# Optimization experiments

Measured on AMD Instinct MI355X. Metric: run time of the kernel, lower is better.

Reference implementation:

```python
import jax, jax.numpy as jnp
import numpy as np

ALPHA = 0.2  # LeakyReLU negative slope


def setup_inputs() -> dict:
    key = jax.random.key(0)
    k1, k2, k3 = jax.random.split(key, 3)
    B, N, F_in, F_out = 8, 2048, 256, 256
    h = jax.random.normal(k1, (B, N, F_in), dtype=jnp.float32)
    adj = jax.random.randint(k2, (B, N, N), 0, 2, dtype=jnp.int32)
    # xavier_uniform for W [F_in, F_out]
    limit = float(np.sqrt(6.0 / (F_in + F_out)))
    W = jax.random.uniform(k3, (F_in, F_out), dtype=jnp.float32, minval=-limit, maxval=limit)
    return {"h": h, "adj": adj, "W": W}


def reference(h, adj, W):
    # h: [B,N,F_in], W: [F_in,F_out] -> Wh: [B,N,F_out]
    Wh = jnp.einsum('bnf,fo->bno', h, W)
    # (Wh_i + Wh_j).sum(-1) == s[p] + s[q] with s = Wh.sum(-1); avoids [B,N,N,F] tensor
    s = Wh.sum(axis=-1)  # [B,N]
    e = jax.nn.leaky_relu(s[:, :, None] + s[:, None, :], negative_slope=ALPHA)  # [B,N,N]
    e = jnp.where(adj == 0, -jnp.inf, e)
    alpha = jax.nn.softmax(e, axis=-1)  # masked softmax over neighbors
    # dropout is identity in eval mode
    h_prime = jnp.einsum('bpq,bqo->bpo', alpha, Wh)  # [B,N,F_out]
    return h_prime
```

## Files before the change

kernel.cpp:

```cpp
#include <hip/hip_runtime.h>
#include <hip/hip_bf16.h>
#include <stdint.h>

#define LEAKY_ALPHA 0.2f

using f32x4 = __attribute__((ext_vector_type(4))) float;
using u32x2 = __attribute__((ext_vector_type(2))) unsigned int;
using u32x4 = __attribute__((ext_vector_type(4))) unsigned int;
using i32x4 = __attribute__((ext_vector_type(4))) int;
using s16x8 = __attribute__((ext_vector_type(8))) short;

static __device__ __forceinline__ unsigned short f2bf(float x) {
  __hip_bfloat16 b = __float2bfloat16(x);
  return __builtin_bit_cast(unsigned short, b);
}

__global__ __launch_bounds__(256) void gat_prep(
    const float* __restrict__ W, __hip_bfloat16* __restrict__ WT,
    float* __restrict__ wsum)
{
  const int o = blockIdx.x;
  const int t = threadIdx.x;
  WT[o * 256 + t] = __float2bfloat16(W[t * 256 + o]);
  float u = W[o * 256 + t];
#pragma unroll
  for (int off = 1; off < 64; off <<= 1) u += __shfl_xor(u, off, 64);
  __shared__ float red[4];
  if ((t & 63) == 0) red[t >> 6] = u;
  __syncthreads();
  if (t == 0) wsum[o] = red[0] + red[1] + red[2] + red[3];
}

__global__ __launch_bounds__(256) void gat_wh2(
    const float* __restrict__ h, const __hip_bfloat16* __restrict__ WT,
    const float* __restrict__ wsum, __hip_bfloat16* __restrict__ WhT,
    float* __restrict__ s)
{
  const int b = blockIdx.x >> 5;
  const int q0 = (blockIdx.x & 31) * 64;
  const int t = threadIdx.x;
  const int wid = t >> 6, lane = t & 63;

  __shared__ __align__(16) unsigned char Bh[64 * 512];
  __shared__ __align__(16) unsigned char Aw[256 * 128];
  __shared__ __align__(16) float wsl[256];

  wsl[t] = wsum[t];
  __syncthreads();

  {
    const int q = t >> 2;
    const int fs = (t & 3) * 64;
    const float* hrow = h + ((size_t)(b * 2048 + q0 + q)) * 256 + fs;
    float sp = 0.f;
#pragma unroll
    for (int c = 0; c < 8; ++c) {
      const f32x4 a  = *(const f32x4*)&hrow[c * 8];
      const f32x4 bq = *(const f32x4*)&hrow[c * 8 + 4];
      const f32x4 wa = *(const f32x4*)&wsl[fs + c * 8];
      const f32x4 wb = *(const f32x4*)&wsl[fs + c * 8 + 4];
      sp += a[0]*wa[0] + a[1]*wa[1] + a[2]*wa[2] + a[3]*wa[3]
          + bq[0]*wb[0] + bq[1]*wb[1] + bq[2]*wb[2] + bq[3]*wb[3];
      u32x4 pk;
      pk[0] = (unsigned)f2bf(a[0])  | ((unsigned)f2bf(a[1])  << 16);
      pk[1] = (unsigned)f2bf(a[2])  | ((unsigned)f2bf(a[3])  << 16);
      pk[2] = (unsigned)f2bf(bq[0]) | ((unsigned)f2bf(bq[1]) << 16);
      pk[3] = (unsigned)f2bf(bq[2]) | ((unsigned)f2bf(bq[3]) << 16);
      const int boff = q * 512 + ((fs * 2 + c * 16) ^ ((q & 7) << 4));
      *(u32x4*)&Bh[boff] = pk;
    }
    sp += __shfl_xor(sp, 1, 64);
    sp += __shfl_xor(sp, 2, 64);
    if ((t & 3) == 0) s[b * 2048 + q0 + q] = sp;
  }

  f32x4 acc[4][4];
#pragma unroll
  for (int i = 0; i < 4; ++i)
#pragma unroll
    for (int j = 0; j < 4; ++j) acc[i][j] = (f32x4)(0.f);

  for (int it = 0; it < 4; ++it) {
    const int f0 = it * 64;
    __syncthreads();
#pragma unroll
    for (int j = 0; j < 8; ++j) {
      const int o = (t >> 3) + 32 * j;
      const int c = t & 7;
      const u32x4 v = *(const u32x4*)&WT[o * 256 + f0 + c * 8];
      *(u32x4*)&Aw[o * 128 + ((c * 16) ^ ((o & 7) << 4))] = v;
    }
    __syncthreads();
#pragma unroll
    for (int kt = 0; kt < 2; ++kt) {
      const int kb = kt * 64 + ((lane >> 4) << 4);
      s16x8 af[4], bf[4];
#pragma unroll
      for (int qt = 0; qt < 4; ++qt) {
        const int qr = qt * 16 + (lane & 15);
        af[qt] = *(const s16x8*)&Bh[qr * 512 + ((f0 * 2 + kb) ^ ((qr & 7) << 4))];
      }
#pragma unroll
      for (int ot = 0; ot < 4; ++ot) {
        const int orow = wid * 64 + ot * 16 + (lane & 15);
        bf[ot] = *(const s16x8*)&Aw[orow * 128 + (kb ^ ((orow & 7) << 4))];
      }
#pragma unroll
      for (int qt = 0; qt < 4; ++qt)
#pragma unroll
        for (int ot = 0; ot < 4; ++ot)
          acc[qt][ot] = __builtin_amdgcn_mfma_f32_16x16x32_bf16(
              af[qt], bf[ot], acc[qt][ot], 0, 0, 0);
    }
  }

  __hip_bfloat16* __restrict__ WhTb = WhT + (size_t)b * 256 * 2048;
#pragma unroll
  for (int qt = 0; qt < 4; ++qt)
#pragma unroll
    for (int ot = 0; ot < 4; ++ot) {
      const int o = wid * 64 + ot * 16 + (lane & 15);
      const int ql = q0 + qt * 16 + ((lane >> 4) << 2);
      u32x2 pk;
      pk[0] = (unsigned)f2bf(acc[qt][ot][0]) | ((unsigned)f2bf(acc[qt][ot][1]) << 16);
      pk[1] = (unsigned)f2bf(acc[qt][ot][2]) | ((unsigned)f2bf(acc[qt][ot][3]) << 16);
      *(u32x2*)&WhTb[(size_t)o * 2048 + ql] = pk;
    }
}

__global__ __launch_bounds__(512, 4) void gat_attn(
    const int* __restrict__ adj, const float* __restrict__ s,
    const __hip_bfloat16* __restrict__ WhT, float* __restrict__ out)
{
  const int N = 2048;
  const int bid = blockIdx.x;
  const int swz = (bid & 7) * 64 + (bid >> 3);
  const int b = swz >> 6;
  const int inner = swz & 63;
  const int p0 = (inner >> 1) * 64;
  const int o0 = (inner & 1) * 128;
  const int t = threadIdx.x;
  const int wid = t >> 6, lane = t & 63;

  __shared__ __align__(16) unsigned char Bs[2][128 * 128];
  __shared__ __align__(16) unsigned char Pt[2][64 * 128];
  __shared__ __align__(16) float red_sh[8];
  __shared__ __align__(16) float l_sh[64];

  const int sp_row = t >> 3;
  const int sq8 = (t & 7) * 8;
  const int* __restrict__ adjrow = adj + ((size_t)(b * N + p0 + sp_row)) * N;
  const float* __restrict__ sB = s + b * N;
  const __hip_bfloat16* __restrict__ WhTb =
      WhT + (size_t)b * 256 * 2048 + (size_t)o0 * 2048;
  const int ptoff = sp_row * 128 + (((t & 7) * 16) ^ ((sp_row & 7) << 4));

  const int so = t >> 3;
  const int q16 = t & 7;

  const int pg = wid >> 2;
  const int og = wid & 3;

  u32x4 breg[2];
#pragma unroll
  for (int c = 0; c < 2; ++c)
    breg[c] = *(const u32x4*)&WhTb[(size_t)(so + 64 * c) * 2048 + q16 * 8];
  i32x4 aE0 = *(const i32x4*)&adjrow[sq8];
  i32x4 aE1 = *(const i32x4*)&adjrow[sq8 + 4];
  f32x4 sE0 = *(const f32x4*)&sB[sq8];
  f32x4 sE1 = *(const f32x4*)&sB[sq8 + 4];
  i32x4 aO0 = *(const i32x4*)&adjrow[64 + sq8];
  i32x4 aO1 = *(const i32x4*)&adjrow[64 + sq8 + 4];
  f32x4 sO0 = *(const f32x4*)&sB[64 + sq8];
  f32x4 sO1 = *(const f32x4*)&sB[64 + sq8 + 4];

  const f32x4 s4 = *(const f32x4*)&sB[t * 4];
  float bm = fmaxf(fmaxf(s4[0], s4[1]), fmaxf(s4[2], s4[3]));
#pragma unroll
  for (int off = 1; off < 64; off <<= 1) bm = fmaxf(bm, __shfl_xor(bm, off, 64));
  if (lane == 0) red_sh[wid] = bm;
  const float s_p = sB[p0 + sp_row];
  __syncthreads();
  float smax = red_sh[0];
#pragma unroll
  for (int k = 1; k < 8; ++k) smax = fmaxf(smax, red_sh[k]);
  const float xm = s_p + smax;
  const float m_p = (xm > 0.f) ? xm : (LEAKY_ALPHA * xm);

  f32x4 acc[2][2];
#pragma unroll
  for (int pt = 0; pt < 2; ++pt)
#pragma unroll
    for (int ot = 0; ot < 2; ++ot) acc[pt][ot] = (f32x4)(0.f);
  float lacc = 0.f;

  auto phase = [&](int BI, int QQ, i32x4& A0, i32x4& A1, f32x4& S0, f32x4& S1)
      __attribute__((always_inline)) {
    float wv[8];
#pragma unroll
    for (int i = 0; i < 4; ++i) {
      const float x = s_p + S0[i];
      const float le = (x > 0.f) ? x : (LEAKY_ALPHA * x);
      const float w = __expf(le - m_p);
      wv[i] = (A0[i] != 0) ? w : 0.f;
      lacc += wv[i];
    }
#pragma unroll
    for (int i = 0; i < 4; ++i) {
      const float x = s_p + S1[i];
      const float le = (x > 0.f) ? x : (LEAKY_ALPHA * x);
      const float w = __expf(le - m_p);
      wv[4 + i] = (A1[i] != 0) ? w : 0.f;
      lacc += wv[4 + i];
    }
    {
      u32x4 pw;
#pragma unroll
      for (int k2 = 0; k2 < 4; ++k2)
        pw[k2] = (unsigned)f2bf(wv[2 * k2]) |
                 ((unsigned)f2bf(wv[2 * k2 + 1]) << 16);
      *(u32x4*)&Pt[BI][ptoff] = pw;
    }
#pragma unroll
    for (int c = 0; c < 2; ++c) {
      const int o = so + 64 * c;
      *(u32x4*)&Bs[BI][o * 128 + ((q16 * 16) ^ ((o & 7) << 4))] = breg[c];
    }
    if (QQ + 64 < N) {
#pragma unroll
      for (int c = 0; c < 2; ++c)
        breg[c] = *(const u32x4*)&WhTb[(size_t)(so + 64 * c) * 2048 +
                                       QQ + 64 + q16 * 8];
    }
    {
      const int qr = (QQ + 128 < N) ? (QQ + 128) : (N - 64);
      A0 = *(const i32x4*)&adjrow[qr + sq8];
      A1 = *(const i32x4*)&adjrow[qr + sq8 + 4];
      S0 = *(const f32x4*)&sB[qr + sq8];
      S1 = *(const f32x4*)&sB[qr + sq8 + 4];
    }
    asm volatile("s_waitcnt lgkmcnt(0)" ::: "memory");
    __builtin_amdgcn_s_barrier();
    asm volatile("" ::: "memory");
    {
      s16x8 afr[2][2], bfr[2][2];
#pragma unroll
      for (int pt = 0; pt < 2; ++pt)
#pragma unroll
        for (int kt = 0; kt < 2; ++kt) {
          const int pa = pg * 32 + pt * 16 + (lane & 15);
          const int kb = kt * 64 + ((lane >> 4) << 4);
          afr[pt][kt] = *(const s16x8*)&Pt[BI][pa * 128 + (kb ^ ((pa & 7) << 4))];
        }
#pragma unroll
      for (int ot = 0; ot < 2; ++ot)
#pragma unroll
        for (int kt = 0; kt < 2; ++kt) {
          const int ob = og * 32 + ot * 16 + (lane & 15);
          const int kb = kt * 64 + ((lane >> 4) << 4);
          bfr[ot][kt] = *(const s16x8*)&Bs[BI][ob * 128 + (kb ^ ((ob & 7) << 4))];
        }
#pragma unroll
      for (int pt = 0; pt < 2; ++pt)
#pragma unroll
        for (int ot = 0; ot < 2; ++ot)
#pragma unroll
          for (int kt = 0; kt < 2; ++kt)
            acc[pt][ot] = __builtin_amdgcn_mfma_f32_16x16x32_bf16(
                afr[pt][kt], bfr[ot][kt], acc[pt][ot], 0, 0, 0);
    }
  };

  for (int q0 = 0; q0 < N; q0 += 128) {
    phase(0, q0, aE0, aE1, sE0, sE1);
    phase(1, q0 + 64, aO0, aO1, sO0, sO1);
  }

  lacc += __shfl_xor(lacc, 1, 64);
  lacc += __shfl_xor(lacc, 2, 64);
  lacc += __shfl_xor(lacc, 4, 64);
  if ((t & 7) == 0) l_sh[sp_row] = lacc;
  __syncthreads();

#pragma unroll
  for (int pt = 0; pt < 2; ++pt) {
    const int pb = pg * 32 + pt * 16 + ((lane >> 4) << 2);
    const f32x4 lv = *(const f32x4*)&l_sh[pb];
    f32x4 inv;
#pragma unroll
    for (int r = 0; r < 4; ++r) inv[r] = 1.f / lv[r];
#pragma unroll
    for (int ot = 0; ot < 2; ++ot) {
      const int o = o0 + og * 32 + ot * 16 + (lane & 15);
#pragma unroll
      for (int r = 0; r < 4; ++r) {
        const int row = p0 + pb + r;
        out[((size_t)(b * N + row)) * 256 + o] = acc[pt][ot][r] * inv[r];
      }
    }
  }
}

extern "C" void kernel_launch(void* const* d_in, const int* in_sizes, int n_in,
                              void* d_out, int out_size, void* d_ws, size_t ws_size,
                              hipStream_t stream) {
  const float* h = (const float*)d_in[0];
  const int* adj = (const int*)d_in[1];
  const float* W = (const float*)d_in[2];
  float* out = (float*)d_out;

  char* ws = (char*)d_ws;
  __hip_bfloat16* WhT = (__hip_bfloat16*)ws;
  float* s = (float*)(ws + (size_t)8 * 1024 * 1024);
  __hip_bfloat16* WT = (__hip_bfloat16*)(ws + (size_t)8 * 1024 * 1024 + 65536);
  float* wsum = (float*)(ws + (size_t)8 * 1024 * 1024 + 65536 + 131072);

  gat_prep<<<256, 256, 0, stream>>>(W, WT, wsum);
  gat_wh2<<<256, 256, 0, stream>>>(h, WT, wsum, WhT, s);
  gat_attn<<<512, 512, 0, stream>>>(adj, s, WhT, out);
}
```

Before: 60.07 us.

## Store Wh in MFMA fragment-major layout and load B operands directly to registers

The projection kernel now writes Wh in a pre-swizzled fragment-major layout, so each lane's MFMA B-operand fragment is a contiguous 16-byte chunk. The attention kernel then loads B fragments straight from global memory into registers, prefetched one step ahead. This removes the shared-memory staging buffer, its stores and its LDS reads. The trade-off is more redundant global/L2 traffic, since each wave loads its own B fragments instead of sharing through LDS, plus higher register pressure.

```diff
diff --git a/kernel.cpp b/kernel.cpp
--- a/kernel.cpp
+++ b/kernel.cpp
@@ -33,7 +33,7 @@
 
 __global__ __launch_bounds__(256) void gat_wh2(
     const float* __restrict__ h, const __hip_bfloat16* __restrict__ WT,
-    const float* __restrict__ wsum, __hip_bfloat16* __restrict__ WhT,
+    const float* __restrict__ wsum, __hip_bfloat16* __restrict__ FM,
     float* __restrict__ s)
 {
   const int b = blockIdx.x >> 5;
@@ -114,23 +114,25 @@
     }
   }
 
-  __hip_bfloat16* __restrict__ WhTb = WhT + (size_t)b * 256 * 2048;
+  char* __restrict__ FMb = (char*)FM + (size_t)b * 1048576;
 #pragma unroll
   for (int qt = 0; qt < 4; ++qt)
 #pragma unroll
     for (int ot = 0; ot < 4; ++ot) {
-      const int o = wid * 64 + ot * 16 + (lane & 15);
-      const int ql = q0 + qt * 16 + ((lane >> 4) << 2);
+      const int i = wid * 4 + ot;
+      const int q = q0 + qt * 16 + ((lane >> 4) << 2);
+      const int c = q >> 5, qq = q & 31;
+      const int lam = (lane & 15) | (((qq >> 3) & 3) << 4);
       u32x2 pk;
       pk[0] = (unsigned)f2bf(acc[qt][ot][0]) | ((unsigned)f2bf(acc[qt][ot][1]) << 16);
       pk[1] = (unsigned)f2bf(acc[qt][ot][2]) | ((unsigned)f2bf(acc[qt][ot][3]) << 16);
-      *(u32x2*)&WhTb[(size_t)o * 2048 + ql] = pk;
+      *(u32x2*)(FMb + ((size_t)(i * 64 + c) * 64 + lam) * 16 + (qq & 4) * 2) = pk;
     }
 }
 
 __global__ __launch_bounds__(512, 4) void gat_attn(
     const int* __restrict__ adj, const float* __restrict__ s,
-    const __hip_bfloat16* __restrict__ WhT, float* __restrict__ out)
+    const __hip_bfloat16* __restrict__ FM, float* __restrict__ out)
 {
   const int N = 2048;
   const int bid = blockIdx.x;
@@ -142,7 +144,6 @@
   const int t = threadIdx.x;
   const int wid = t >> 6, lane = t & 63;
 
-  __shared__ __align__(16) unsigned char Bs[2][128 * 128];
   __shared__ __align__(16) unsigned char Pt[2][64 * 128];
   __shared__ __align__(16) float red_sh[8];
   __shared__ __align__(16) float l_sh[64];
@@ -151,20 +152,21 @@
   const int sq8 = (t & 7) * 8;
   const int* __restrict__ adjrow = adj + ((size_t)(b * N + p0 + sp_row)) * N;
   const float* __restrict__ sB = s + b * N;
-  const __hip_bfloat16* __restrict__ WhTb =
-      WhT + (size_t)b * 256 * 2048 + (size_t)o0 * 2048;
   const int ptoff = sp_row * 128 + (((t & 7) * 16) ^ ((sp_row & 7) << 4));
-
-  const int so = t >> 3;
-  const int q16 = t & 7;
 
   const int pg = wid >> 2;
   const int og = wid & 3;
-
-  u32x4 breg[2];
-#pragma unroll
-  for (int c = 0; c < 2; ++c)
-    breg[c] = *(const u32x4*)&WhTb[(size_t)(so + 64 * c) * 2048 + q16 * 8];
+  const int ibase = (o0 >> 4) + og * 2;
+  const char* __restrict__ FMb = (const char*)FM + (size_t)b * 1048576 + lane * 16;
+
+  u32x4 bE[2][2], bO[2][2];
+#pragma unroll
+  for (int ot = 0; ot < 2; ++ot)
+#pragma unroll
+    for (int kt = 0; kt < 2; ++kt) {
+      bE[ot][kt] = *(const u32x4*)(FMb + ((size_t)((ibase + ot) * 64 + kt) * 1024));
+      bO[ot][kt] = *(const u32x4*)(FMb + ((size_t)((ibase + ot) * 64 + 2 + kt) * 1024));
+    }
   i32x4 aE0 = *(const i32x4*)&adjrow[sq8];
   i32x4 aE1 = *(const i32x4*)&adjrow[sq8 + 4];
   f32x4 sE0 = *(const f32x4*)&sB[sq8];
@@ -194,8 +196,8 @@
     for (int ot = 0; ot < 2; ++ot) acc[pt][ot] = (f32x4)(0.f);
   float lacc = 0.f;
 
-  auto phase = [&](int BI, int QQ, i32x4& A0, i32x4& A1, f32x4& S0, f32x4& S1)
-      __attribute__((always_inline)) {
+  auto phase = [&](int BI, int QQ, i32x4& A0, i32x4& A1, f32x4& S0, f32x4& S1,
+                   u32x4 (&BF)[2][2]) __attribute__((always_inline)) {
     float wv[8];
 #pragma unroll
     for (int i = 0; i < 4; ++i) {
@@ -221,17 +223,6 @@
                  ((unsigned)f2bf(wv[2 * k2 + 1]) << 16);
       *(u32x4*)&Pt[BI][ptoff] = pw;
     }
-#pragma unroll
-    for (int c = 0; c < 2; ++c) {
-      const int o = so + 64 * c;
-      *(u32x4*)&Bs[BI][o * 128 + ((q16 * 16) ^ ((o & 7) << 4))] = breg[c];
-    }
-    if (QQ + 64 < N) {
-#pragma unroll
-      for (int c = 0; c < 2; ++c)
-        breg[c] = *(const u32x4*)&WhTb[(size_t)(so + 64 * c) * 2048 +
-                                       QQ + 64 + q16 * 8];
-    }
     {
       const int qr = (QQ + 128 < N) ? (QQ + 128) : (N - 64);
       A0 = *(const i32x4*)&adjrow[qr + sq8];
@@ -243,7 +234,7 @@
     __builtin_amdgcn_s_barrier();
     asm volatile("" ::: "memory");
     {
-      s16x8 afr[2][2], bfr[2][2];
+      s16x8 afr[2][2];
 #pragma unroll
       for (int pt = 0; pt < 2; ++pt)
 #pragma unroll
@@ -253,27 +244,29 @@
           afr[pt][kt] = *(const s16x8*)&Pt[BI][pa * 128 + (kb ^ ((pa & 7) << 4))];
         }
 #pragma unroll
-      for (int ot = 0; ot < 2; ++ot)
-#pragma unroll
-        for (int kt = 0; kt < 2; ++kt) {
-          const int ob = og * 32 + ot * 16 + (lane & 15);
-          const int kb = kt * 64 + ((lane >> 4) << 4);
-          bfr[ot][kt] = *(const s16x8*)&Bs[BI][ob * 128 + (kb ^ ((ob & 7) << 4))];
-        }
-#pragma unroll
       for (int pt = 0; pt < 2; ++pt)
 #pragma unroll
         for (int ot = 0; ot < 2; ++ot)
 #pragma unroll
           for (int kt = 0; kt < 2; ++kt)
             acc[pt][ot] = __builtin_amdgcn_mfma_f32_16x16x32_bf16(
-                afr[pt][kt], bfr[ot][kt], acc[pt][ot], 0, 0, 0);
+                afr[pt][kt], __builtin_bit_cast(s16x8, BF[ot][kt]),
+                acc[pt][ot], 0, 0, 0);
+    }
+    {
+      const int cr = ((QQ + 128 < N) ? (QQ + 128) : (N - 64)) >> 5;
+#pragma unroll
+      for (int ot = 0; ot < 2; ++ot)
+#pragma unroll
+        for (int kt = 0; kt < 2; ++kt)
+          BF[ot][kt] = *(const u32x4*)(FMb +
+              ((size_t)((ibase + ot) * 64 + cr + kt) * 1024));
     }
   };
 
   for (int q0 = 0; q0 < N; q0 += 128) {
-    phase(0, q0, aE0, aE1, sE0, sE1);
-    phase(1, q0 + 64, aO0, aO1, sO0, sO1);
+    phase(0, q0, aE0, aE1, sE0, sE1, bE);
+    phase(1, q0 + 64, aO0, aO1, sO0, sO1, bO);
   }
 
   lacc += __shfl_xor(lacc, 1, 64);
@@ -310,12 +303,12 @@
   float* out = (float*)d_out;
 
   char* ws = (char*)d_ws;
-  __hip_bfloat16* WhT = (__hip_bfloat16*)ws;
+  __hip_bfloat16* FM = (__hip_bfloat16*)ws;
   float* s = (float*)(ws + (size_t)8 * 1024 * 1024);
   __hip_bfloat16* WT = (__hip_bfloat16*)(ws + (size_t)8 * 1024 * 1024 + 65536);
   float* wsum = (float*)(ws + (size_t)8 * 1024 * 1024 + 65536 + 131072);
 
   gat_prep<<<256, 256, 0, stream>>>(W, WT, wsum);
-  gat_wh2<<<256, 256, 0, stream>>>(h, WT, wsum, WhT, s);
-  gat_attn<<<512, 512, 0, stream>>>(adj, s, WhT, out);
-}
+  gat_wh2<<<256, 256, 0, stream>>>(h, WT, wsum, FM, s);
+  gat_attn<<<512, 512, 0, stream>>>(adj, s, FM, out);
+}
```

After: 63.66 us. +6.0%, slower.
